# Performance work log

Hardware: AMD Instinct MI355X
Metric: run time of the kernel (lower is better)

The kernel has to match this reference:

```python
import jax, jax.numpy as jnp
import numpy as np

L0, L1, L2 = 32, 16, 8          # multiplicities of 0e, 1o, 2e irreps
NS = 128                        # numscalars
NB = 64                         # numbasis
CUTOFF = 7.0
N_NODES = 50000
N_EDGES = 400000
N_GRAPH = 32
NODE_DIM = L0 + 3 * L1 + 5 * L2  # 120


def setup_inputs() -> dict:
    key = jax.random.key(0)
    ks = jax.random.split(key, 16)
    return {
        "nodes": jax.random.normal(ks[0], (N_NODES, NODE_DIM), jnp.float32),
        "edge_index": jax.random.randint(ks[1], (2, N_EDGES), 0, N_NODES),
        "graph_batch": jnp.sort(jax.random.randint(ks[2], (N_NODES,), 0, N_GRAPH)),
        "cell": jax.random.normal(ks[3], (N_GRAPH, 3, 3), jnp.float32),
        "edge_shift": jax.random.normal(ks[4], (N_EDGES, 3), jnp.float32),
        "pos": jax.random.normal(ks[5], (N_NODES, 3), jnp.float32),
        # FullyConnectedTensorProduct weights: one uvw block per (l,l)->0e path
        "W0": jax.random.normal(ks[6], (L0, L0, NS), jnp.float32),
        "W1": jax.random.normal(ks[7], (L1, L1, NS), jnp.float32),
        "W2": jax.random.normal(ks[8], (L2, L2, NS), jnp.float32),
        "ln_g": jnp.ones((NS,), jnp.float32),
        "ln_b": jnp.zeros((NS,), jnp.float32),
        "df_w1": jax.random.normal(ks[9], (NB, 128), jnp.float32) / np.sqrt(NB).astype(np.float32),
        "df_b1": jnp.zeros((128,), jnp.float32),
        "df_w2": jax.random.normal(ks[10], (128, NS), jnp.float32) / np.sqrt(128.0).astype(np.float32),
        "df_b2": jnp.zeros((NS,), jnp.float32),
        "mlp_w1": jax.random.normal(ks[11], (NS, 512), jnp.float32) / np.sqrt(NS).astype(np.float32),
        "mlp_b1": jnp.zeros((512,), jnp.float32),
        "mlp_w2": jax.random.normal(ks[12], (512, 1), jnp.float32) / np.sqrt(512.0).astype(np.float32),
        "mlp_b2": jnp.zeros((1,), jnp.float32),
    }


def _split_irreps(x):
    # x: [E, L0 + 3*L1 + 5*L2] -> scalar / vector / rank-2 blocks
    a = x[:, :L0]                                   # [E, L0]    0e
    b = x[:, L0:L0 + 3 * L1].reshape(-1, L1, 3)     # [E, L1, 3] 1o
    c = x[:, L0 + 3 * L1:].reshape(-1, L2, 5)       # [E, L2, 5] 2e
    return a, b, c


def _tensor_product(x1, x2, W0, W1, W2):
    # e3nn FullyConnectedTensorProduct to {NS}x0e: only (l,l)->0 paths survive.
    # Real-basis wigner_3j(l,l,0) = I / sqrt(2l+1); 'element' path norm with
    # scalar output gives alpha = 1 / (L0^2 + L1^2 + L2^2) shared by all paths.
    a1, b1, c1 = _split_irreps(x1)
    a2, b2, c2 = _split_irreps(x2)
    alpha = 1.0 / np.sqrt(float(L0 * L0 + L1 * L1 + L2 * L2))
    out = (jnp.einsum('eu,ev,uvw->ew', a1, a2, W0)
           + jnp.einsum('eum,evm,uvw->ew', b1, b2, W1) * (1.0 / np.sqrt(3.0))
           + jnp.einsum('eum,evm,uvw->ew', c1, c2, W2) * (1.0 / np.sqrt(5.0)))
    return jnp.asarray(alpha, out.dtype) * out


def reference(nodes, edge_index, graph_batch, cell, edge_shift, pos,
              W0, W1, W2, ln_g, ln_b, df_w1, df_b1, df_w2, df_b2,
              mlp_w1, mlp_b1, mlp_w2, mlp_b2):
    src, dst = edge_index[0], edge_index[1]
    bcell = cell[graph_batch[src]]                            # [E,3,3]
    tvec = jnp.einsum('ei,eij->ej', edge_shift, bcell)        # [E,3]
    radvec = pos[dst] - pos[src] + tvec
    dist = jnp.linalg.norm(radvec, axis=1, keepdims=True)     # [E,1]

    mixed = _tensor_product(nodes[src], nodes[dst], W0, W1, W2)  # [E,NS]
    mu = jnp.mean(mixed, axis=-1, keepdims=True)
    var = jnp.mean((mixed - mu) ** 2, axis=-1, keepdims=True)
    mixednorm = (mixed - mu) / jnp.sqrt(var + 1e-5) * ln_g + ln_b

    # RadialEmbedding: Gaussian RBF * cosine envelope with hard cutoff
    offset = jnp.linspace(0.0, CUTOFF, NB).astype(dist.dtype)
    width = CUTOFF / (NB - 1)
    coeff = -0.5 / (width * width)
    rbf = jnp.exp(coeff * (dist - offset[None, :]) ** 2)      # [E,NB]
    env = 0.5 * (jnp.cos(dist * jnp.pi / CUTOFF) + 1.0)
    env = env * (dist < CUTOFF).astype(dist.dtype)            # [E,1]
    demb = rbf * env

    dfilter = jax.nn.silu(demb @ df_w1 + df_b1) @ df_w2 + df_b2  # [E,NS]
    regulated = mixednorm * dfilter
    out = jax.nn.silu(regulated @ mlp_w1 + mlp_b1) @ mlp_w2 + mlp_b2  # [E,1]
    return out
```

## Files before the change

kernel.cpp:

```cpp
#include <hip/hip_runtime.h>
#include <hip/hip_bf16.h>
#include <math.h>

typedef unsigned short ushort_t;
typedef short short8 __attribute__((ext_vector_type(8)));
typedef short short4v __attribute__((ext_vector_type(4)));
typedef float f32x4 __attribute__((ext_vector_type(4)));

#define E_TOTAL 400000
#define ET 32
#define NTHR 512
#define NODE_D 120
#define XSTR 124
#define PSTR 520
#define HSTR 136
#define DSTR 72

#define ALPHA 0.0272772362793f
#define S_L1  0.57735026918962f
#define S_L2  0.44721359549996f

#define WS_WF1 172032
#define WS_WF2 180224
#define WS_WM1 196608
#define WS_TOTAL 262144

__device__ __forceinline__ ushort_t f2b(float f) {
    unsigned int b = __float_as_uint(f);
    b += 0x7FFFu + ((b >> 16) & 1u);
    return (ushort_t)(b >> 16);
}
__device__ __forceinline__ float silu_f(float x) { return x / (1.0f + __expf(-x)); }

__global__ __launch_bounds__(256) void prep_weights(
    const float* __restrict__ W0, const float* __restrict__ W1, const float* __restrict__ W2,
    const float* __restrict__ df_w1, const float* __restrict__ df_w2,
    const float* __restrict__ mlp_w1, ushort_t* __restrict__ ws)
{
    const int i = blockIdx.x * 256 + threadIdx.x;
    if (i >= WS_TOTAL) return;
    float v;
    if (i < WS_WF1) {
        const int r = i;
        const int kt = r >> 12, nt = (r >> 9) & 7, l = (r >> 3) & 63, jj = r & 7;
        const int k = kt * 32 + ((l >> 4) << 3) + jj;
        const int n = nt * 16 + (l & 15);
        if (k < 1024)      v = W0[k * 128 + n] * ALPHA;
        else if (k < 1280) v = W1[(k - 1024) * 128 + n] * (ALPHA * S_L1);
        else               v = W2[(k - 1280) * 128 + n] * (ALPHA * S_L2);
    } else if (i < WS_WF2) {
        const int r = i - WS_WF1;
        const int kt = r >> 12, nt = (r >> 9) & 7, l = (r >> 3) & 63, jj = r & 7;
        v = df_w1[(kt * 32 + ((l >> 4) << 3) + jj) * 128 + nt * 16 + (l & 15)];
    } else if (i < WS_WM1) {
        const int r = i - WS_WF2;
        const int kt = r >> 12, nt = (r >> 9) & 7, l = (r >> 3) & 63, jj = r & 7;
        v = df_w2[(kt * 32 + ((l >> 4) << 3) + jj) * 128 + nt * 16 + (l & 15)];
    } else {
        const int r = i - WS_WM1;
        const int kt = r >> 14, nt = (r >> 9) & 31, l = (r >> 3) & 63, jj = r & 7;
        v = mlp_w1[(kt * 32 + ((l >> 4) << 3) + jj) * 512 + nt * 16 + (l & 15)];
    }
    ws[i] = f2b(v);
}

__device__ __forceinline__ void build_l0(ushort_t* __restrict__ P,
                                         const float* __restrict__ x1,
                                         const float* __restrict__ x2,
                                         int tid, int ubase)
{
    const int e = tid >> 4, uu = tid & 15;
    const float a1u = x1[e * XSTR + ubase + uu];
    f32x4 a2v[8];
#pragma unroll
    for (int q = 0; q < 8; ++q) a2v[q] = *(const f32x4*)(x2 + e * XSTR + q * 4);
    ushort_t tmp[32];
#pragma unroll
    for (int q = 0; q < 8; ++q) {
        tmp[q * 4 + 0] = f2b(a1u * a2v[q][0]);
        tmp[q * 4 + 1] = f2b(a1u * a2v[q][1]);
        tmp[q * 4 + 2] = f2b(a1u * a2v[q][2]);
        tmp[q * 4 + 3] = f2b(a1u * a2v[q][3]);
    }
    ushort_t* dst = P + e * PSTR + uu * 32;
#pragma unroll
    for (int q = 0; q < 4; ++q)
        *(short8*)(dst + q * 8) = *(const short8*)(tmp + q * 8);
}

__global__ __launch_bounds__(NTHR, 4) void fused_edge_kernel(
    const float* __restrict__ nodes, const int* __restrict__ edge_index,
    const int* __restrict__ graph_batch, const float* __restrict__ cell,
    const float* __restrict__ edge_shift, const float* __restrict__ pos,
    const float* __restrict__ ln_g, const float* __restrict__ ln_b,
    const float* __restrict__ df_b1, const float* __restrict__ df_b2,
    const float* __restrict__ mlp_b1, const float* __restrict__ mlp_w2,
    const float* __restrict__ mlp_b2,
    const ushort_t* __restrict__ wsp, float* __restrict__ out)
{
    __shared__ __align__(16) ushort_t P[ET * PSTR];
    __shared__ __align__(16) float xbuf[2 * ET * XSTR];
    __shared__ __align__(16) ushort_t demb[ET * DSTR];
    __shared__ float dist_s[ET];
    __shared__ int sidx[ET], didx[ET];
    __shared__ float mu_s[ET], rstd_s[ET];

    float* x1 = xbuf;
    float* x2 = xbuf + ET * XSTR;
    ushort_t* h1   = (ushort_t*)xbuf;
    ushort_t* regb = (ushort_t*)xbuf + ET * HSTR;
    float* red1 = (float*)((char*)xbuf + 17408);
    float* red2 = (float*)((char*)xbuf + 19456);

    const int tid = threadIdx.x;
    const int e0g = blockIdx.x * ET;
    const int wave = tid >> 6, lane = tid & 63;
    const int lr = lane & 15, lg = lane >> 4;

    if (tid < ET) {
        const int e = e0g + tid;
        const int s = edge_index[e];
        const int d = edge_index[E_TOTAL + e];
        sidx[tid] = s; didx[tid] = d;
        const int g = graph_batch[s];
        const float* c = cell + g * 9;
        const float sx = edge_shift[e * 3], sy = edge_shift[e * 3 + 1], sz = edge_shift[e * 3 + 2];
        const float t0 = sx * c[0] + sy * c[3] + sz * c[6];
        const float t1 = sx * c[1] + sy * c[4] + sz * c[7];
        const float t2 = sx * c[2] + sy * c[5] + sz * c[8];
        const float r0 = pos[d * 3 + 0] - pos[s * 3 + 0] + t0;
        const float r1 = pos[d * 3 + 1] - pos[s * 3 + 1] + t1;
        const float r2 = pos[d * 3 + 2] - pos[s * 3 + 2] + t2;
        dist_s[tid] = sqrtf(r0 * r0 + r1 * r1 + r2 * r2);
    }
    __syncthreads();

    for (int i = tid; i < ET * 32; i += NTHR) {
        const int e = i >> 5, c = i & 31;
        if (c < 30)
            *(float4*)(x1 + e * XSTR + c * 4) = *(const float4*)(nodes + (size_t)sidx[e] * NODE_D + c * 4);
    }
    for (int i = tid; i < ET * 32; i += NTHR) {
        const int e = i >> 5, c = i & 31;
        if (c < 30)
            *(float4*)(x2 + e * XSTR + c * 4) = *(const float4*)(nodes + (size_t)didx[e] * NODE_D + c * 4);
    }
    for (int i = tid; i < ET * 64; i += NTHR) {
        const int e = i >> 6, k = i & 63;
        const float d = dist_s[e];
        const float t = d - (7.0f / 63.0f) * (float)k;
        const float rbf = __expf(-40.5f * t * t);
        const float env = (d < 7.0f) ? (0.5f * (__cosf(d * (3.14159265358979f / 7.0f)) + 1.0f)) : 0.0f;
        demb[e * DSTR + k] = f2b(rbf * env);
    }
    __syncthreads();

    const char* pA0 = (const char*)P + lr * (PSTR * 2) + lg * 16;
    const char* pA1 = pA0 + 16 * (PSTR * 2);
    const short8* WT8 = (const short8*)wsp;
    const int bcol = wave * 64 + lane;

    f32x4 acc0 = {0.f, 0.f, 0.f, 0.f}, acc1 = {0.f, 0.f, 0.f, 0.f};

    build_l0(P, x1, x2, tid, 0);
    __syncthreads();
#pragma unroll 4
    for (int kt = 0; kt < 16; ++kt) {
        const short8 a0 = *(const short8*)(pA0 + kt * 64);
        const short8 a1 = *(const short8*)(pA1 + kt * 64);
        const short8 b = WT8[kt * 512 + bcol];
        acc0 = __builtin_amdgcn_mfma_f32_16x16x32_bf16(a0, b, acc0, 0, 0, 0);
        acc1 = __builtin_amdgcn_mfma_f32_16x16x32_bf16(a1, b, acc1, 0, 0, 0);
    }
    __syncthreads();

    build_l0(P, x1, x2, tid, 16);
    __syncthreads();
#pragma unroll 4
    for (int kt = 0; kt < 16; ++kt) {
        const short8 a0 = *(const short8*)(pA0 + kt * 64);
        const short8 a1 = *(const short8*)(pA1 + kt * 64);
        const short8 b = WT8[(16 + kt) * 512 + bcol];
        acc0 = __builtin_amdgcn_mfma_f32_16x16x32_bf16(a0, b, acc0, 0, 0, 0);
        acc1 = __builtin_amdgcn_mfma_f32_16x16x32_bf16(a1, b, acc1, 0, 0, 0);
    }
    __syncthreads();

    {
        const int e = tid >> 4, t = tid & 15;
        const float* b1p = x1 + e * XSTR + 32 + 3 * t;
        const float b1a = b1p[0], b1b = b1p[1], b1c = b1p[2];
        ushort_t tmp[16];
#pragma unroll
        for (int v = 0; v < 16; ++v) {
            const float* b2p = x2 + e * XSTR + 32 + 3 * v;
            tmp[v] = f2b(b1a * b2p[0] + b1b * b2p[1] + b1c * b2p[2]);
        }
        ushort_t* dst = P + e * PSTR + t * 16;
        *(short8*)(dst)     = *(const short8*)(tmp);
        *(short8*)(dst + 8) = *(const short8*)(tmp + 8);
        ushort_t t2[4];
#pragma unroll
        for (int q = 0; q < 4; ++q) {
            const int p = 4 * t + q, u = p >> 3, v = p & 7;
            const float* c1p = x1 + e * XSTR + 80 + 5 * u;
            const float* c2p = x2 + e * XSTR + 80 + 5 * v;
            t2[q] = f2b(c1p[0] * c2p[0] + c1p[1] * c2p[1] + c1p[2] * c2p[2]
                      + c1p[3] * c2p[3] + c1p[4] * c2p[4]);
        }
        *(short4v*)(P + e * PSTR + 256 + t * 4) = *(const short4v*)(t2);
    }
    __syncthreads();

#pragma unroll 2
    for (int kt = 0; kt < 10; ++kt) {
        const short8 a0 = *(const short8*)(pA0 + kt * 64);
        const short8 a1 = *(const short8*)(pA1 + kt * 64);
        const short8 b = WT8[(32 + kt) * 512 + bcol];
        acc0 = __builtin_amdgcn_mfma_f32_16x16x32_bf16(a0, b, acc0, 0, 0, 0);
        acc1 = __builtin_amdgcn_mfma_f32_16x16x32_bf16(a1, b, acc1, 0, 0, 0);
    }
    {
        f32x4 f0 = {0.f, 0.f, 0.f, 0.f}, f1 = {0.f, 0.f, 0.f, 0.f};
        const char* dA0 = (const char*)demb + lr * (DSTR * 2) + lg * 16;
        const char* dA1 = dA0 + 16 * (DSTR * 2);
#pragma unroll
        for (int kt = 0; kt < 2; ++kt) {
            const short8 a0 = *(const short8*)(dA0 + kt * 64);
            const short8 a1 = *(const short8*)(dA1 + kt * 64);
            const short8 b = WT8[WS_WF1 / 8 + kt * 512 + bcol];
            f0 = __builtin_amdgcn_mfma_f32_16x16x32_bf16(a0, b, f0, 0, 0, 0);
            f1 = __builtin_amdgcn_mfma_f32_16x16x32_bf16(a1, b, f1, 0, 0, 0);
        }
        const int n = wave * 16 + lr;
        const float bb = df_b1[n];
#pragma unroll
        for (int r = 0; r < 4; ++r) {
            h1[(lg * 4 + r) * HSTR + n]        = f2b(silu_f(f0[r] + bb));
            h1[(16 + lg * 4 + r) * HSTR + n]   = f2b(silu_f(f1[r] + bb));
        }
    }
    __syncthreads();

    f32x4 d0 = {0.f, 0.f, 0.f, 0.f}, d1 = {0.f, 0.f, 0.f, 0.f};
    {
        const char* hA0 = (const char*)h1 + lr * (HSTR * 2) + lg * 16;
        const char* hA1 = hA0 + 16 * (HSTR * 2);
#pragma unroll
        for (int kt = 0; kt < 4; ++kt) {
            const short8 a0 = *(const short8*)(hA0 + kt * 64);
            const short8 a1 = *(const short8*)(hA1 + kt * 64);
            const short8 b = WT8[WS_WF2 / 8 + kt * 512 + bcol];
            d0 = __builtin_amdgcn_mfma_f32_16x16x32_bf16(a0, b, d0, 0, 0, 0);
            d1 = __builtin_amdgcn_mfma_f32_16x16x32_bf16(a1, b, d1, 0, 0, 0);
        }
        const int n = wave * 16 + lr;
        const float b2v = df_b2[n];
#pragma unroll
        for (int r = 0; r < 4; ++r) { d0[r] += b2v; d1[r] += b2v; }
    }

#pragma unroll
    for (int mt = 0; mt < 2; ++mt) {
#pragma unroll
        for (int r = 0; r < 4; ++r) {
            const float v = mt ? acc1[r] : acc0[r];
            float s1 = v, s2 = v * v;
            s1 += __shfl_xor(s1, 1);  s2 += __shfl_xor(s2, 1);
            s1 += __shfl_xor(s1, 2);  s2 += __shfl_xor(s2, 2);
            s1 += __shfl_xor(s1, 4);  s2 += __shfl_xor(s2, 4);
            s1 += __shfl_xor(s1, 8);  s2 += __shfl_xor(s2, 8);
            if (lr == 0) {
                const int idx = ((wave * 2 + mt) * 4 + lg) * 4 + r;
                red1[idx] = s1;
                red1[256 + idx] = s2;
            }
        }
    }
    __syncthreads();
    if (tid < ET) {
        const int mt = tid >> 4, g = (tid >> 2) & 3, r = tid & 3;
        float s1 = 0.f, s2 = 0.f;
#pragma unroll
        for (int w = 0; w < 8; ++w) {
            const int idx = ((w * 2 + mt) * 4 + g) * 4 + r;
            s1 += red1[idx];
            s2 += red1[256 + idx];
        }
        const float mu = s1 * (1.0f / 128.0f);
        const float var = s2 * (1.0f / 128.0f) - mu * mu;
        mu_s[tid] = mu;
        rstd_s[tid] = rsqrtf(var + 1e-5f);
    }
    __syncthreads();

    {
        const int n = wave * 16 + lr;
        const float gv = ln_g[n], bv = ln_b[n];
#pragma unroll
        for (int mt = 0; mt < 2; ++mt) {
#pragma unroll
            for (int r = 0; r < 4; ++r) {
                const int row = mt * 16 + lg * 4 + r;
                const float v = mt ? acc1[r] : acc0[r];
                const float ln = (v - mu_s[row]) * rstd_s[row] * gv + bv;
                const float df = mt ? d1[r] : d0[r];
                regb[row * HSTR + n] = f2b(ln * df);
            }
        }
    }
    __syncthreads();

    {
        f32x4 m00 = {0.f,0.f,0.f,0.f}, m01 = {0.f,0.f,0.f,0.f};
        f32x4 m10 = {0.f,0.f,0.f,0.f}, m11 = {0.f,0.f,0.f,0.f};
        f32x4 m20 = {0.f,0.f,0.f,0.f}, m21 = {0.f,0.f,0.f,0.f};
        f32x4 m30 = {0.f,0.f,0.f,0.f}, m31 = {0.f,0.f,0.f,0.f};
        const char* rA0 = (const char*)regb + lr * (HSTR * 2) + lg * 16;
        const char* rA1 = rA0 + 16 * (HSTR * 2);
#pragma unroll
        for (int kt = 0; kt < 4; ++kt) {
            const short8 a0 = *(const short8*)(rA0 + kt * 64);
            const short8 a1 = *(const short8*)(rA1 + kt * 64);
            const int base = WS_WM1 / 8 + kt * 2048 + wave * 256 + lane;
            const short8 b0 = WT8[base];
            const short8 b1 = WT8[base + 64];
            const short8 b2 = WT8[base + 128];
            const short8 b3 = WT8[base + 192];
            m00 = __builtin_amdgcn_mfma_f32_16x16x32_bf16(a0, b0, m00, 0, 0, 0);
            m01 = __builtin_amdgcn_mfma_f32_16x16x32_bf16(a1, b0, m01, 0, 0, 0);
            m10 = __builtin_amdgcn_mfma_f32_16x16x32_bf16(a0, b1, m10, 0, 0, 0);
            m11 = __builtin_amdgcn_mfma_f32_16x16x32_bf16(a1, b1, m11, 0, 0, 0);
            m20 = __builtin_amdgcn_mfma_f32_16x16x32_bf16(a0, b2, m20, 0, 0, 0);
            m21 = __builtin_amdgcn_mfma_f32_16x16x32_bf16(a1, b2, m21, 0, 0, 0);
            m30 = __builtin_amdgcn_mfma_f32_16x16x32_bf16(a0, b3, m30, 0, 0, 0);
            m31 = __builtin_amdgcn_mfma_f32_16x16x32_bf16(a1, b3, m31, 0, 0, 0);
        }
        float po0[4] = {0.f,0.f,0.f,0.f}, po1[4] = {0.f,0.f,0.f,0.f};
#pragma unroll
        for (int q = 0; q < 4; ++q) {
            const int n = (wave * 4 + q) * 16 + lr;
            const float b1v = mlp_b1[n];
            const float w2v = mlp_w2[n];
            const f32x4 h0 = (q == 0) ? m00 : (q == 1) ? m10 : (q == 2) ? m20 : m30;
            const f32x4 h1v = (q == 0) ? m01 : (q == 1) ? m11 : (q == 2) ? m21 : m31;
#pragma unroll
            for (int r = 0; r < 4; ++r) {
                po0[r] += silu_f(h0[r] + b1v) * w2v;
                po1[r] += silu_f(h1v[r] + b1v) * w2v;
            }
        }
#pragma unroll
        for (int r = 0; r < 4; ++r) {
            float a = po0[r], b = po1[r];
            a += __shfl_xor(a, 1); b += __shfl_xor(b, 1);
            a += __shfl_xor(a, 2); b += __shfl_xor(b, 2);
            a += __shfl_xor(a, 4); b += __shfl_xor(b, 4);
            a += __shfl_xor(a, 8); b += __shfl_xor(b, 8);
            if (lr == 0) {
                red2[((wave * 2 + 0) * 4 + lg) * 4 + r] = a;
                red2[((wave * 2 + 1) * 4 + lg) * 4 + r] = b;
            }
        }
    }
    __syncthreads();
    if (tid < ET) {
        const int mt = tid >> 4, g = (tid >> 2) & 3, r = tid & 3;
        float s = 0.f;
#pragma unroll
        for (int w = 0; w < 8; ++w)
            s += red2[((w * 2 + mt) * 4 + g) * 4 + r];
        out[e0g + tid] = s + mlp_b2[0];
    }
}

extern "C" void kernel_launch(void* const* d_in, const int* in_sizes, int n_in,
                              void* d_out, int out_size, void* d_ws, size_t ws_size,
                              hipStream_t stream) {
    const float* nodes      = (const float*)d_in[0];
    const int*   edge_index = (const int*)  d_in[1];
    const int*   graph_b    = (const int*)  d_in[2];
    const float* cell       = (const float*)d_in[3];
    const float* edge_shift = (const float*)d_in[4];
    const float* pos        = (const float*)d_in[5];
    const float* W0         = (const float*)d_in[6];
    const float* W1         = (const float*)d_in[7];
    const float* W2         = (const float*)d_in[8];
    const float* ln_g       = (const float*)d_in[9];
    const float* ln_b       = (const float*)d_in[10];
    const float* df_w1      = (const float*)d_in[11];
    const float* df_b1      = (const float*)d_in[12];
    const float* df_w2      = (const float*)d_in[13];
    const float* df_b2      = (const float*)d_in[14];
    const float* mlp_w1     = (const float*)d_in[15];
    const float* mlp_b1     = (const float*)d_in[16];
    const float* mlp_w2     = (const float*)d_in[17];
    const float* mlp_b2     = (const float*)d_in[18];
    float* out = (float*)d_out;
    ushort_t* ws = (ushort_t*)d_ws;

    hipLaunchKernelGGL(prep_weights, dim3((WS_TOTAL + 255) / 256), dim3(256), 0, stream,
                       W0, W1, W2, df_w1, df_w2, mlp_w1, ws);

    const int E = in_sizes[1] / 2;
    const int grid = E / ET;
    hipLaunchKernelGGL(fused_edge_kernel, dim3(grid), dim3(NTHR), 0, stream,
                       nodes, edge_index, graph_b, cell, edge_shift, pos,
                       ln_g, ln_b, df_b1, df_b2, mlp_b1, mlp_w2, mlp_b2,
                       ws, out);
}
```

Baseline: 536.2 us.

## Store MFMA A-operands in fragment-native LDS layout with packed bf16 conversion

Every LDS buffer that feeds MFMA A operands (outer-product P, radial embedding, hidden h1, regulated features) now uses a fragment-major layout. Each lane then reads its 16-byte short8 with a contiguous lane*16 address instead of a padded row-stride pattern. The builders are reorganised so each thread writes one full uint4 fragment, using paired float2-to-bf16 conversion. The aim is fewer LDS bank conflicts, a smaller LDS footprint and cheaper conversions, at the cost of more complex index math and scattered 2-byte stores for h1 and the regulated features.

After: 509.4 us. -5.0%, faster.

```diff
diff --git a/kernel.cpp b/kernel.cpp
--- a/kernel.cpp
+++ b/kernel.cpp
@@ -4,7 +4,6 @@
 
 typedef unsigned short ushort_t;
 typedef short short8 __attribute__((ext_vector_type(8)));
-typedef short short4v __attribute__((ext_vector_type(4)));
 typedef float f32x4 __attribute__((ext_vector_type(4)));
 
 #define E_TOTAL 400000
@@ -12,9 +11,6 @@
 #define NTHR 512
 #define NODE_D 120
 #define XSTR 124
-#define PSTR 520
-#define HSTR 136
-#define DSTR 72
 
 #define ALPHA 0.0272772362793f
 #define S_L1  0.57735026918962f
@@ -29,6 +25,11 @@
     unsigned int b = __float_as_uint(f);
     b += 0x7FFFu + ((b >> 16) & 1u);
     return (ushort_t)(b >> 16);
+}
+__device__ __forceinline__ unsigned int f2b2(float a, float b) {
+    __hip_bfloat162 h = __float22bfloat162_rn(make_float2(a, b));
+    union { __hip_bfloat162 h2; unsigned int u; } cv; cv.h2 = h;
+    return cv.u;
 }
 __device__ __forceinline__ float silu_f(float x) { return x / (1.0f + __expf(-x)); }
 
@@ -64,28 +65,32 @@
     ws[i] = f2b(v);
 }
 
-__device__ __forceinline__ void build_l0(ushort_t* __restrict__ P,
-                                         const float* __restrict__ x1,
-                                         const float* __restrict__ x2,
-                                         int tid, int ubase)
+__device__ __forceinline__ void build_l0_frag(ushort_t* __restrict__ Pf,
+                                              const float* __restrict__ x1,
+                                              const float* __restrict__ x2,
+                                              int tid, int ubase)
 {
-    const int e = tid >> 4, uu = tid & 15;
-    const float a1u = x1[e * XSTR + ubase + uu];
-    f32x4 a2v[8];
-#pragma unroll
-    for (int q = 0; q < 8; ++q) a2v[q] = *(const f32x4*)(x2 + e * XSTR + q * 4);
-    ushort_t tmp[32];
-#pragma unroll
-    for (int q = 0; q < 8; ++q) {
-        tmp[q * 4 + 0] = f2b(a1u * a2v[q][0]);
-        tmp[q * 4 + 1] = f2b(a1u * a2v[q][1]);
-        tmp[q * 4 + 2] = f2b(a1u * a2v[q][2]);
-        tmp[q * 4 + 3] = f2b(a1u * a2v[q][3]);
-    }
-    ushort_t* dst = P + e * PSTR + uu * 32;
-#pragma unroll
-    for (int q = 0; q < 4; ++q)
-        *(short8*)(dst + q * 8) = *(const short8*)(tmp + q * 8);
+    const int er = tid & 15, kg = (tid >> 4) & 3, w = tid >> 6;
+#pragma unroll
+    for (int half = 0; half < 2; ++half) {
+        const int e = half * 16 + er;
+        const float* x2r = x2 + e * XSTR + kg * 8;
+        const float2 xv0 = *(const float2*)(x2r + 0);
+        const float2 xv1 = *(const float2*)(x2r + 2);
+        const float2 xv2 = *(const float2*)(x2r + 4);
+        const float2 xv3 = *(const float2*)(x2r + 6);
+#pragma unroll
+        for (int uu = 0; uu < 2; ++uu) {
+            const int ul = w + uu * 8;
+            const float a1 = x1[e * XSTR + ubase + ul];
+            uint4 o;
+            o.x = f2b2(a1 * xv0.x, a1 * xv0.y);
+            o.y = f2b2(a1 * xv1.x, a1 * xv1.y);
+            o.z = f2b2(a1 * xv2.x, a1 * xv2.y);
+            o.w = f2b2(a1 * xv3.x, a1 * xv3.y);
+            *(uint4*)(Pf + ((ul * 2 + half) * 64 + kg * 16 + er) * 8) = o;
+        }
+    }
 }
 
 __global__ __launch_bounds__(NTHR, 4) void fused_edge_kernel(
@@ -98,19 +103,19 @@
     const float* __restrict__ mlp_b2,
     const ushort_t* __restrict__ wsp, float* __restrict__ out)
 {
-    __shared__ __align__(16) ushort_t P[ET * PSTR];
+    __shared__ __align__(16) ushort_t Pf[16 * 2 * 64 * 8];
     __shared__ __align__(16) float xbuf[2 * ET * XSTR];
-    __shared__ __align__(16) ushort_t demb[ET * DSTR];
+    __shared__ __align__(16) ushort_t dembF[2 * 2 * 64 * 8];
     __shared__ float dist_s[ET];
     __shared__ int sidx[ET], didx[ET];
     __shared__ float mu_s[ET], rstd_s[ET];
 
     float* x1 = xbuf;
     float* x2 = xbuf + ET * XSTR;
-    ushort_t* h1   = (ushort_t*)xbuf;
-    ushort_t* regb = (ushort_t*)xbuf + ET * HSTR;
-    float* red1 = (float*)((char*)xbuf + 17408);
-    float* red2 = (float*)((char*)xbuf + 19456);
+    ushort_t* h1F  = (ushort_t*)xbuf;
+    ushort_t* regF = (ushort_t*)xbuf + 4096;
+    float* red1 = (float*)((char*)xbuf + 16384);
+    float* red2 = (float*)((char*)xbuf + 18432);
 
     const int tid = threadIdx.x;
     const int e0g = blockIdx.x * ET;
@@ -151,35 +156,35 @@
         const float t = d - (7.0f / 63.0f) * (float)k;
         const float rbf = __expf(-40.5f * t * t);
         const float env = (d < 7.0f) ? (0.5f * (__cosf(d * (3.14159265358979f / 7.0f)) + 1.0f)) : 0.0f;
-        demb[e * DSTR + k] = f2b(rbf * env);
-    }
-    __syncthreads();
-
-    const char* pA0 = (const char*)P + lr * (PSTR * 2) + lg * 16;
-    const char* pA1 = pA0 + 16 * (PSTR * 2);
+        const int ktl = k >> 5, kg = (k >> 3) & 3, jj = k & 7, half = e >> 4, row = e & 15;
+        dembF[((ktl * 2 + half) * 64 + kg * 16 + row) * 8 + jj] = f2b(rbf * env);
+    }
+    __syncthreads();
+
+    const char* pA = (const char*)Pf + lane * 16;
     const short8* WT8 = (const short8*)wsp;
     const int bcol = wave * 64 + lane;
 
     f32x4 acc0 = {0.f, 0.f, 0.f, 0.f}, acc1 = {0.f, 0.f, 0.f, 0.f};
 
-    build_l0(P, x1, x2, tid, 0);
+    build_l0_frag(Pf, x1, x2, tid, 0);
     __syncthreads();
 #pragma unroll 4
     for (int kt = 0; kt < 16; ++kt) {
-        const short8 a0 = *(const short8*)(pA0 + kt * 64);
-        const short8 a1 = *(const short8*)(pA1 + kt * 64);
+        const short8 a0 = *(const short8*)(pA + kt * 2048);
+        const short8 a1 = *(const short8*)(pA + kt * 2048 + 1024);
         const short8 b = WT8[kt * 512 + bcol];
         acc0 = __builtin_amdgcn_mfma_f32_16x16x32_bf16(a0, b, acc0, 0, 0, 0);
         acc1 = __builtin_amdgcn_mfma_f32_16x16x32_bf16(a1, b, acc1, 0, 0, 0);
     }
     __syncthreads();
 
-    build_l0(P, x1, x2, tid, 16);
+    build_l0_frag(Pf, x1, x2, tid, 16);
     __syncthreads();
 #pragma unroll 4
     for (int kt = 0; kt < 16; ++kt) {
-        const short8 a0 = *(const short8*)(pA0 + kt * 64);
-        const short8 a1 = *(const short8*)(pA1 + kt * 64);
+        const short8 a0 = *(const short8*)(pA + kt * 2048);
+        const short8 a1 = *(const short8*)(pA + kt * 2048 + 1024);
         const short8 b = WT8[(16 + kt) * 512 + bcol];
         acc0 = __builtin_amdgcn_mfma_f32_16x16x32_bf16(a0, b, acc0, 0, 0, 0);
         acc1 = __builtin_amdgcn_mfma_f32_16x16x32_bf16(a1, b, acc1, 0, 0, 0);
@@ -187,69 +192,85 @@
     __syncthreads();
 
     {
-        const int e = tid >> 4, t = tid & 15;
-        const float* b1p = x1 + e * XSTR + 32 + 3 * t;
-        const float b1a = b1p[0], b1b = b1p[1], b1c = b1p[2];
-        ushort_t tmp[16];
-#pragma unroll
-        for (int v = 0; v < 16; ++v) {
-            const float* b2p = x2 + e * XSTR + 32 + 3 * v;
-            tmp[v] = f2b(b1a * b2p[0] + b1b * b2p[1] + b1c * b2p[2]);
-        }
-        ushort_t* dst = P + e * PSTR + t * 16;
-        *(short8*)(dst)     = *(const short8*)(tmp);
-        *(short8*)(dst + 8) = *(const short8*)(tmp + 8);
-        ushort_t t2[4];
-#pragma unroll
-        for (int q = 0; q < 4; ++q) {
-            const int p = 4 * t + q, u = p >> 3, v = p & 7;
-            const float* c1p = x1 + e * XSTR + 80 + 5 * u;
-            const float* c2p = x2 + e * XSTR + 80 + 5 * v;
-            t2[q] = f2b(c1p[0] * c2p[0] + c1p[1] * c2p[1] + c1p[2] * c2p[2]
-                      + c1p[3] * c2p[3] + c1p[4] * c2p[4]);
-        }
-        *(short4v*)(P + e * PSTR + 256 + t * 4) = *(const short4v*)(t2);
+        const int er = tid & 15, kg = (tid >> 4) & 3, w = tid >> 6;
+        const int u1 = 2 * w + (kg >> 1);
+        const int vb = (kg & 1) * 8;
+#pragma unroll
+        for (int half = 0; half < 2; ++half) {
+            const int e = half * 16 + er;
+            const float* b1p = x1 + e * XSTR + 32 + 3 * u1;
+            const float b1a = b1p[0], b1b = b1p[1], b1c = b1p[2];
+            const float* b2b = x2 + e * XSTR + 32 + 3 * vb;
+            float pr[8];
+#pragma unroll
+            for (int jj = 0; jj < 8; ++jj) {
+                const float* b2p = b2b + 3 * jj;
+                pr[jj] = b1a * b2p[0] + b1b * b2p[1] + b1c * b2p[2];
+            }
+            uint4 o;
+            o.x = f2b2(pr[0], pr[1]); o.y = f2b2(pr[2], pr[3]);
+            o.z = f2b2(pr[4], pr[5]); o.w = f2b2(pr[6], pr[7]);
+            *(uint4*)(Pf + ((w * 2 + half) * 64 + lane) * 8) = o;
+        }
+        if (w < 4) {
+            const int half = w & 1;
+            const int ktl = 8 + (w >> 1);
+            const int u2 = (ktl - 8) * 4 + kg;
+            const int e = half * 16 + er;
+            const float* c1p = x1 + e * XSTR + 80 + 5 * u2;
+            const float c1a = c1p[0], c1b = c1p[1], c1c = c1p[2], c1d = c1p[3], c1e = c1p[4];
+            float pr[8];
+#pragma unroll
+            for (int jj = 0; jj < 8; ++jj) {
+                const float* c2p = x2 + e * XSTR + 80 + 5 * jj;
+                pr[jj] = c1a * c2p[0] + c1b * c2p[1] + c1c * c2p[2] + c1d * c2p[3] + c1e * c2p[4];
+            }
+            uint4 o;
+            o.x = f2b2(pr[0], pr[1]); o.y = f2b2(pr[2], pr[3]);
+            o.z = f2b2(pr[4], pr[5]); o.w = f2b2(pr[6], pr[7]);
+            *(uint4*)(Pf + ((ktl * 2 + half) * 64 + lane) * 8) = o;
+        }
     }
     __syncthreads();
 
 #pragma unroll 2
     for (int kt = 0; kt < 10; ++kt) {
-        const short8 a0 = *(const short8*)(pA0 + kt * 64);
-        const short8 a1 = *(const short8*)(pA1 + kt * 64);
+        const short8 a0 = *(const short8*)(pA + kt * 2048);
+        const short8 a1 = *(const short8*)(pA + kt * 2048 + 1024);
         const short8 b = WT8[(32 + kt) * 512 + bcol];
         acc0 = __builtin_amdgcn_mfma_f32_16x16x32_bf16(a0, b, acc0, 0, 0, 0);
         acc1 = __builtin_amdgcn_mfma_f32_16x16x32_bf16(a1, b, acc1, 0, 0, 0);
     }
     {
         f32x4 f0 = {0.f, 0.f, 0.f, 0.f}, f1 = {0.f, 0.f, 0.f, 0.f};
-        const char* dA0 = (const char*)demb + lr * (DSTR * 2) + lg * 16;
-        const char* dA1 = dA0 + 16 * (DSTR * 2);
+        const char* dA = (const char*)dembF + lane * 16;
 #pragma unroll
         for (int kt = 0; kt < 2; ++kt) {
-            const short8 a0 = *(const short8*)(dA0 + kt * 64);
-            const short8 a1 = *(const short8*)(dA1 + kt * 64);
+            const short8 a0 = *(const short8*)(dA + kt * 2048);
+            const short8 a1 = *(const short8*)(dA + kt * 2048 + 1024);
             const short8 b = WT8[WS_WF1 / 8 + kt * 512 + bcol];
             f0 = __builtin_amdgcn_mfma_f32_16x16x32_bf16(a0, b, f0, 0, 0, 0);
             f1 = __builtin_amdgcn_mfma_f32_16x16x32_bf16(a1, b, f1, 0, 0, 0);
         }
         const int n = wave * 16 + lr;
         const float bb = df_b1[n];
+        const int ktl = n >> 5, kg2 = (n >> 3) & 3, jj = n & 7;
 #pragma unroll
         for (int r = 0; r < 4; ++r) {
-            h1[(lg * 4 + r) * HSTR + n]        = f2b(silu_f(f0[r] + bb));
-            h1[(16 + lg * 4 + r) * HSTR + n]   = f2b(silu_f(f1[r] + bb));
+            const int row = lg * 4 + r;
+            h1F[((ktl * 2 + 0) * 64 + kg2 * 16 + row) * 8 + jj] = f2b(silu_f(f0[r] + bb));
+            h1F[((ktl * 2 + 1) * 64 + kg2 * 16 + row) * 8 + jj] = f2b(silu_f(f1[r] + bb));
         }
     }
     __syncthreads();
 
     f32x4 d0 = {0.f, 0.f, 0.f, 0.f}, d1 = {0.f, 0.f, 0.f, 0.f};
     {
-        const char* hA0 = (const char*)h1 + lr * (HSTR * 2) + lg * 16;
-        const char* hA1 = hA0 + 16 * (HSTR * 2);
+        const char* hA = (const char*)h1F + lane * 16;
 #pragma unroll
         for (int kt = 0; kt < 4; ++kt) {
-            const short8 a0 = *(const short8*)(hA0 + kt * 64);
-            const short8 a1 = *(const short8*)(hA1 + kt * 64);
+            const short8 a0 = *(const short8*)(hA + kt * 2048);
+            const short8 a1 = *(const short8*)(hA + kt * 2048 + 1024);
             const short8 b = WT8[WS_WF2 / 8 + kt * 512 + bcol];
             d0 = __builtin_amdgcn_mfma_f32_16x16x32_bf16(a0, b, d0, 0, 0, 0);
             d1 = __builtin_amdgcn_mfma_f32_16x16x32_bf16(a1, b, d1, 0, 0, 0);
@@ -259,7 +280,6 @@
 #pragma unroll
         for (int r = 0; r < 4; ++r) { d0[r] += b2v; d1[r] += b2v; }
     }
-
 #pragma unroll
     for (int mt = 0; mt < 2; ++mt) {
 #pragma unroll
@@ -297,15 +317,16 @@
     {
         const int n = wave * 16 + lr;
         const float gv = ln_g[n], bv = ln_b[n];
+        const int ktl = n >> 5, kg2 = (n >> 3) & 3, jj = n & 7;
 #pragma unroll
         for (int mt = 0; mt < 2; ++mt) {
 #pragma unroll
             for (int r = 0; r < 4; ++r) {
-                const int row = mt * 16 + lg * 4 + r;
+                const int row = lg * 4 + r;
                 const float v = mt ? acc1[r] : acc0[r];
-                const float ln = (v - mu_s[row]) * rstd_s[row] * gv + bv;
+                const float ln = (v - mu_s[mt * 16 + row]) * rstd_s[mt * 16 + row] * gv + bv;
                 const float df = mt ? d1[r] : d0[r];
-                regb[row * HSTR + n] = f2b(ln * df);
+                regF[((ktl * 2 + mt) * 64 + kg2 * 16 + row) * 8 + jj] = f2b(ln * df);
             }
         }
     }
@@ -316,12 +337,11 @@
         f32x4 m10 = {0.f,0.f,0.f,0.f}, m11 = {0.f,0.f,0.f,0.f};
         f32x4 m20 = {0.f,0.f,0.f,0.f}, m21 = {0.f,0.f,0.f,0.f};
         f32x4 m30 = {0.f,0.f,0.f,0.f}, m31 = {0.f,0.f,0.f,0.f};
-        const char* rA0 = (const char*)regb + lr * (HSTR * 2) + lg * 16;
-        const char* rA1 = rA0 + 16 * (HSTR * 2);
+        const char* rA = (const char*)regF + lane * 16;
 #pragma unroll
         for (int kt = 0; kt < 4; ++kt) {
-            const short8 a0 = *(const short8*)(rA0 + kt * 64);
-            const short8 a1 = *(const short8*)(rA1 + kt * 64);
+            const short8 a0 = *(const short8*)(rA + kt * 2048);
+            const short8 a1 = *(const short8*)(rA + kt * 2048 + 1024);
             const int base = WS_WM1 / 8 + kt * 2048 + wave * 256 + lane;
             const short8 b0 = WT8[base];
             const short8 b1 = WT8[base + 64];
```
